# Performance work log

Hardware: AMD Instinct MI355X
Metric: run time of the kernel (lower is better)

Reference implementation:

```python
import jax, jax.numpy as jnp
import numpy as np

R = 0.2          # stable-distribution hash bucket width
TABLE_SIZE = 2   # hash table size (buckets)
M = 5            # number of appended ALSH transform dims
EPS = 1e-12


def conv2d(x, W, b, pad):
    out = jax.lax.conv_general_dilated(
        x, W, window_strides=(1, 1), padding=[(pad, pad), (pad, pad)],
        dimension_numbers=('NCHW', 'OIHW', 'NCHW'))
    return out + b[None, :, None, None]


def maxpool2(x):
    return jax.lax.reduce_window(x, -jnp.inf, jax.lax.max,
                                 (1, 1, 2, 2), (1, 1, 2, 2), 'VALID')


def alsh_mask(x, W, a, c):
    """ALSH filter selection: hash P(kernels) and Q(query) with a stable
    distribution hash h(v)=floor((a.v+b)/r) mod table_size; active filters
    are those landing in the query's bucket. Returns [B, Cout] 0/1 mask.
    Multiplying conv output by this mask == gather active filters then
    zero_fill_missing back to full channel count."""
    Cout, Cin, kH, kW = W.shape
    Kf = W.reshape(Cout, -1)                       # [Cout, Cin*kH*kW]
    norms = jnp.linalg.norm(Kf, axis=1)
    Kn = Kf / (jnp.max(norms) + EPS)               # scale so all norms <= 1
    n = jnp.linalg.norm(Kn, axis=1, keepdims=True)
    # P transform: append norm^2, norm^4, ..., norm^(2^M)
    powers = jnp.concatenate([n ** (2 ** (i + 1)) for i in range(M)], axis=1)
    P = jnp.concatenate([Kn, powers], axis=1)      # [Cout, d+M]
    kh = jnp.mod(jnp.floor((P @ a + c[0]) / R), TABLE_SIZE)  # [Cout]
    # query vector: per-sample channel means broadcast over kernel support
    cm = x.mean(axis=(2, 3))                       # [B, Cin]
    q = jnp.repeat(cm, kH * kW, axis=1)            # [B, Cin*kH*kW] (cin,kh,kw order)
    qn = q / (jnp.linalg.norm(q, axis=1, keepdims=True) + EPS)
    # Q transform: append M halves
    Qv = jnp.concatenate([qn, jnp.full((q.shape[0], M), 0.5, q.dtype)], axis=1)
    qh = jnp.mod(jnp.floor((Qv @ a + c[0]) / R), TABLE_SIZE)  # [B]
    return (kh[None, :] == qh[:, None]).astype(x.dtype)       # [B, Cout]


def setup_inputs() -> dict:
    key = jax.random.key(0)
    ks = jax.random.split(key, 16)
    u = lambda k, s: jax.random.uniform(k, s, jnp.float32, 0.0, R)
    n = lambda k, s, sc=0.1: jax.random.normal(k, s, jnp.float32) * sc
    return {
        'x': jax.random.normal(ks[0], (4096, 3, 32, 32), jnp.float32),
        'W1': n(ks[1], (16, 3, 5, 5)), 'b1': n(ks[2], (16,)),
        'a1': jax.random.normal(ks[3], (80,), jnp.float32), 'c1': u(ks[4], (1,)),
        'W2': n(ks[5], (20, 16, 5, 5)), 'b2': n(ks[6], (20,)),
        'a2': jax.random.normal(ks[7], (405,), jnp.float32), 'c2': u(ks[8], (1,)),
        'W3': n(ks[9], (20, 20, 5, 5)), 'b3': n(ks[10], (20,)),
        'a3': jax.random.normal(ks[11], (505,), jnp.float32), 'c3': u(ks[12], (1,)),
        'Wo': n(ks[13], (10, 320)), 'bo': n(ks[14], (10,)),
    }


def reference(x, W1, b1, a1, c1, W2, b2, a2, c2, W3, b3, a3, c3, Wo, bo):
    m1 = alsh_mask(x, W1, a1, c1)
    h = jax.nn.relu(conv2d(x, W1, b1, 2)) * m1[:, :, None, None]
    h = maxpool2(h)                                # [B,16,16,16]
    m2 = alsh_mask(h, W2, a2, c2)
    h = jax.nn.relu(conv2d(h, W2, b2, 2)) * m2[:, :, None, None]
    h = maxpool2(h)                                # [B,20,8,8]
    m3 = alsh_mask(h, W3, a3, c3)
    h = jax.nn.relu(conv2d(h, W3, b3, 2)) * m3[:, :, None, None]
    # zero_fill_missing -> identity here: inactive channels already zero
    h = maxpool2(h)                                # [B,20,4,4]
    flat = h.reshape(h.shape[0], -1)               # [B,320]
    return flat @ Wo.T + bo
```

## Files before the change

### kernel.cpp

```cpp
#include <hip/hip_runtime.h>
#include <hip/hip_bf16.h>

#define EPSV 1e-12
#define RHASH 0.2

__device__ __forceinline__ int fmod2(double t) {
    return (int)(((long long)floor(t)) & 1LL);
}

__device__ __forceinline__ void load_row6(const float* base, float* r) {
    float2 a0 = *(const float2*)(base);
    float2 a1 = *(const float2*)(base + 2);
    float2 a2 = *(const float2*)(base + 4);
    r[0] = a0.x; r[1] = a0.y; r[2] = a1.x; r[3] = a1.y; r[4] = a2.x; r[5] = a2.y;
}

__device__ void layer_setup(const float* W, const float* a, double cval,
                            int Co, int Ci, int* kh, double* asum, double* qc,
                            double* s_norm, float* Wbuf, float* abuf)
{
    const int t = threadIdx.x;
    const int D = Ci * 25;
    for (int i = t; i < Co * D; i += 256) Wbuf[i] = W[i];
    for (int i = t; i < D + 5; i += 256) abuf[i] = a[i];
    __syncthreads();
    if (t < Co) {
        double s = 0;
        for (int j = 0; j < D; ++j) { double w = (double)Wbuf[t * D + j]; s += w * w; }
        s_norm[t] = sqrt(s);
    }
    __syncthreads();
    if (t == 0) {
        double mx = 0;
        for (int i = 0; i < Co; ++i) mx = fmax(mx, s_norm[i]);
        s_norm[23] = 1.0 / (mx + EPSV);
    }
    __syncthreads();
    double scale = s_norm[23];
    if (t < Co) {
        double dp = 0;
        for (int j = 0; j < D; ++j) dp += (double)Wbuf[t * D + j] * (double)abuf[j];
        dp *= scale;
        double n = s_norm[t] * scale;
        double p = n * n;
        for (int m = 0; m < 5; ++m) { dp += p * (double)abuf[D + m]; p *= p; }
        kh[t] = fmod2((dp + cval) / RHASH);
    }
    if (t >= 64 && t < 64 + Ci) {
        int c = t - 64;
        double s = 0;
        for (int j = 0; j < 25; ++j) s += (double)abuf[c * 25 + j];
        asum[c] = s;
    }
    if (t == 128) {
        double s = 0;
        for (int m = 0; m < 5; ++m) s += (double)abuf[D + m];
        *qc = 0.5 * s + cval;
    }
    __syncthreads();
}

__global__ __launch_bounds__(256) void setup_kernel(
    const float* W1, const float* a1, const float* c1,
    const float* W2, const float* a2, const float* c2,
    const float* W3, const float* a3, const float* c3,
    double* dmeta, int* imeta)
{
    __shared__ float Wbuf[10000];
    __shared__ float abuf[512];
    __shared__ double s_norm[24];
    layer_setup(W1, a1, (double)c1[0], 16, 3,  imeta + 0,  dmeta + 0,  dmeta + 39, s_norm, Wbuf, abuf);
    layer_setup(W2, a2, (double)c2[0], 20, 16, imeta + 16, dmeta + 3,  dmeta + 40, s_norm, Wbuf, abuf);
    layer_setup(W3, a3, (double)c3[0], 20, 20, imeta + 36, dmeta + 19, dmeta + 41, s_norm, Wbuf, abuf);
}

__global__ __launch_bounds__(256) void pack_kernel(const float* W1, const float* W2, const float* W3,
                                                   float* Wp1, float* Wp2, float* Wp3)
{
    int i = blockIdx.x * 256 + threadIdx.x;
    if (i < 1200) {
        int co = i & 15, r = i >> 4;
        int kx = r % 5, r2 = r / 5, ky = r2 % 5, ci = r2 / 5;
        Wp1[i] = W1[co * 75 + ci * 25 + ky * 5 + kx];
    } else if (i < 1200 + 8960) {
        int k = i - 1200;
        int j = k % 28, r = k / 28;
        int cog = r % 4, r2 = r / 4, ky = r2 % 5, ci = r2 / 5;
        Wp2[k] = (j < 25) ? W2[(cog * 5 + j / 5) * 400 + ci * 25 + ky * 5 + (j % 5)] : 0.f;
    } else if (i < 1200 + 8960 + 11200) {
        int k = i - 10160;
        int j = k % 28, r = k / 28;
        int cog = r % 4, r2 = r / 4, ky = r2 % 5, ci = r2 / 5;
        Wp3[k] = (j < 25) ? W3[(cog * 5 + j / 5) * 500 + ci * 25 + ky * 5 + (j % 5)] : 0.f;
    }
}

__global__ __launch_bounds__(256) void conv1_kernel(
    const float* __restrict__ x, const float* __restrict__ Wp1,
    const float* __restrict__ b1, const int* __restrict__ kh1,
    const double* __restrict__ dmeta, float* __restrict__ h1,
    int* __restrict__ qh2)
{
    __shared__ float xs[3][36][38];
    __shared__ float Ws[1200];
    __shared__ double s_red[3];
    __shared__ double s_ch[16][4];

    const int b = blockIdx.x, t = threadIdx.x;
    const int w = t >> 6, ln = t & 63;

    for (int i = t; i < 3 * 36 * 38; i += 256) (&xs[0][0][0])[i] = 0.f;
    for (int i = t; i < 600; i += 256) ((float2*)Ws)[i] = ((const float2*)Wp1)[i];
    __syncthreads();
    const float2* xb2 = (const float2*)(x + (size_t)b * 3072);
    for (int i = t; i < 1536; i += 256) {
        int idx = i * 2, c = idx >> 10, rem = idx & 1023;
        *(float2*)&xs[c][(rem >> 5) + 2][(rem & 31) + 2] = xb2[i];
    }
    __syncthreads();

    if (w < 3) {
        double s = 0;
        for (int j = 0; j < 16; ++j) {
            int i = ln + 64 * j;
            s += (double)xs[w][(i >> 5) + 2][(i & 31) + 2];
        }
        #pragma unroll
        for (int off = 32; off; off >>= 1) s += __shfl_xor(s, off);
        if (ln == 0) s_red[w] = s;
    }
    __syncthreads();
    double dp = 0, nn = 0;
    #pragma unroll
    for (int c = 0; c < 3; ++c) {
        double cm = s_red[c] * (1.0 / 1024.0);
        dp += cm * dmeta[c]; nn += cm * cm;
    }
    const int qh = fmod2((dp / (5.0 * sqrt(nn) + EPSV) + dmeta[39]) / RHASH);

    const int py = t >> 4, px = t & 15;
    const int y0 = 2 * py, x0 = 2 * px;

    float acc[16][4];
    #pragma unroll
    for (int c = 0; c < 16; ++c) {
        float bb = b1[c];
        acc[c][0] = bb; acc[c][1] = bb; acc[c][2] = bb; acc[c][3] = bb;
    }
    #pragma unroll
    for (int ci = 0; ci < 3; ++ci) {
        float cur[6], nxt[6];
        load_row6(&xs[ci][y0][x0], cur);
        load_row6(&xs[ci][y0 + 1][x0], nxt);
        #pragma unroll
        for (int ky = 0; ky < 5; ++ky) {
            const float* wbase = Ws + ((ci * 5 + ky) * 5) * 16;
            #pragma unroll
            for (int kx = 0; kx < 5; ++kx) {
                float wc[16];
                const float4* wp = (const float4*)(wbase + kx * 16);
                *(float4*)&wc[0]  = wp[0];
                *(float4*)&wc[4]  = wp[1];
                *(float4*)&wc[8]  = wp[2];
                *(float4*)&wc[12] = wp[3];
                #pragma unroll
                for (int c = 0; c < 16; ++c) {
                    acc[c][0] = fmaf(wc[c], cur[kx],     acc[c][0]);
                    acc[c][1] = fmaf(wc[c], cur[kx + 1], acc[c][1]);
                    acc[c][2] = fmaf(wc[c], nxt[kx],     acc[c][2]);
                    acc[c][3] = fmaf(wc[c], nxt[kx + 1], acc[c][3]);
                }
            }
            if (ky < 4) {
                #pragma unroll
                for (int j = 0; j < 6; ++j) cur[j] = nxt[j];
                load_row6(&xs[ci][y0 + ky + 2][x0], nxt);
            }
        }
    }

    float mv[16];
    float* hb = h1 + (size_t)b * 4096 + t;
    #pragma unroll
    for (int c = 0; c < 16; ++c) {
        float m = fmaxf(fmaxf(acc[c][0], acc[c][1]), fmaxf(acc[c][2], acc[c][3]));
        mv[c] = fmaxf(m, 0.f) * ((kh1[c] == qh) ? 1.f : 0.f);
        hb[c * 256] = mv[c];
    }
    #pragma unroll
    for (int c = 0; c < 16; ++c) {
        double s = (double)mv[c];
        #pragma unroll
        for (int off = 32; off; off >>= 1) s += __shfl_xor(s, off);
        if (ln == 0) s_ch[c][w] = s;
    }
    __syncthreads();
    if (t == 0) {
        double dp2 = 0, nn2 = 0;
        #pragma unroll
        for (int c = 0; c < 16; ++c) {
            double cm = (s_ch[c][0] + s_ch[c][1] + s_ch[c][2] + s_ch[c][3]) * (1.0 / 256.0);
            dp2 += cm * dmeta[3 + c]; nn2 += cm * cm;
        }
        qh2[b] = fmod2((dp2 / (5.0 * sqrt(nn2) + EPSV) + dmeta[40]) / RHASH);
    }
}

__global__ __launch_bounds__(256) void conv2_kernel(
    const float* __restrict__ h1, const float* __restrict__ Wp2,
    const float* __restrict__ b2, const int* __restrict__ kh2,
    const int* __restrict__ qh2, const double* __restrict__ dmeta,
    float* __restrict__ h2, int* __restrict__ qh3)
{
    __shared__ float xs[8][20][22];
    __shared__ float Ws[4480];
    __shared__ double s_ch[20];

    const int b = blockIdx.x, t = threadIdx.x;
    const int cog = t >> 6, pos = t & 63;
    const int py = pos >> 3, px = pos & 7;
    const int y0 = 2 * py, x0 = 2 * px;

    for (int i = t; i < 8 * 20 * 22; i += 256) (&xs[0][0][0])[i] = 0.f;

    const int qh = qh2[b];
    float acc[5][4];
    #pragma unroll
    for (int c = 0; c < 5; ++c) {
        float bb = b2[cog * 5 + c];
        acc[c][0] = bb; acc[c][1] = bb; acc[c][2] = bb; acc[c][3] = bb;
    }
    __syncthreads();

    for (int ch = 0; ch < 2; ++ch) {
        for (int i = t; i < 2240; i += 256)
            ((float2*)Ws)[i] = ((const float2*)(Wp2 + ch * 4480))[i];
        const float2* src = (const float2*)(h1 + (size_t)b * 4096 + ch * 2048);
        for (int i = t; i < 1024; i += 256) {
            int ci = i >> 7, r = i & 127, p2 = r * 2;
            *(float2*)&xs[ci][(p2 >> 4) + 2][(p2 & 15) + 2] = src[i];
        }
        __syncthreads();

        for (int ci = 0; ci < 8; ++ci) {
            float cur[6], nxt[6];
            load_row6(&xs[ci][y0][x0], cur);
            load_row6(&xs[ci][y0 + 1][x0], nxt);
            #pragma unroll
            for (int ky = 0; ky < 5; ++ky) {
                float wv[28];
                const float4* wp = (const float4*)&Ws[((ci * 5 + ky) * 4 + cog) * 28];
                *(float4*)&wv[0]  = wp[0];
                *(float4*)&wv[4]  = wp[1];
                *(float4*)&wv[8]  = wp[2];
                *(float4*)&wv[12] = wp[3];
                *(float4*)&wv[16] = wp[4];
                *(float4*)&wv[20] = wp[5];
                *(float4*)&wv[24] = wp[6];
                #pragma unroll
                for (int c = 0; c < 5; ++c) {
                    #pragma unroll
                    for (int kx = 0; kx < 5; ++kx) {
                        float wgt = wv[c * 5 + kx];
                        acc[c][0] = fmaf(wgt, cur[kx],     acc[c][0]);
                        acc[c][1] = fmaf(wgt, cur[kx + 1], acc[c][1]);
                        acc[c][2] = fmaf(wgt, nxt[kx],     acc[c][2]);
                        acc[c][3] = fmaf(wgt, nxt[kx + 1], acc[c][3]);
                    }
                }
                if (ky < 4) {
                    #pragma unroll
                    for (int j = 0; j < 6; ++j) cur[j] = nxt[j];
                    load_row6(&xs[ci][y0 + ky + 2][x0], nxt);
                }
            }
        }
        __syncthreads();
    }

    float mv[5];
    float* ob = h2 + (size_t)b * 1280 + pos;
    #pragma unroll
    for (int c = 0; c < 5; ++c) {
        int co = cog * 5 + c;
        float m = fmaxf(fmaxf(acc[c][0], acc[c][1]), fmaxf(acc[c][2], acc[c][3]));
        mv[c] = fmaxf(m, 0.f) * ((kh2[co] == qh) ? 1.f : 0.f);
        ob[co * 64] = mv[c];
    }
    #pragma unroll
    for (int c = 0; c < 5; ++c) {
        double s = (double)mv[c];
        #pragma unroll
        for (int off = 32; off; off >>= 1) s += __shfl_xor(s, off);
        if (pos == 0) s_ch[cog * 5 + c] = s;
    }
    __syncthreads();
    if (t == 0) {
        double dp = 0, nn = 0;
        #pragma unroll
        for (int c = 0; c < 20; ++c) {
            double cm = s_ch[c] * (1.0 / 64.0);
            dp += cm * dmeta[19 + c]; nn += cm * cm;
        }
        qh3[b] = fmod2((dp / (5.0 * sqrt(nn) + EPSV) + dmeta[41]) / RHASH);
    }
}

__global__ __launch_bounds__(256) void conv3_kernel(
    const float* __restrict__ h2, const float* __restrict__ Wp3,
    const float* __restrict__ b3, const int* __restrict__ kh3,
    const int* __restrict__ qh3,
    const float* __restrict__ Wo, const float* __restrict__ bo,
    float* __restrict__ out, int B)
{
    __shared__ float xs[4][5][12][14];
    __shared__ float Ws[2800];
    __shared__ float flat[4][320];

    const int b0 = blockIdx.x * 4, t = threadIdx.x;
    const int s = t >> 6, q = t & 63, cog = q >> 4, pos = q & 15;
    const int py = pos >> 2, px = pos & 3;
    const int y0 = 2 * py, x0 = 2 * px;
    const int b = b0 + s;

    for (int i = t; i < 4 * 5 * 12 * 14; i += 256) (&xs[0][0][0][0])[i] = 0.f;

    const int qh = (b < B) ? qh3[b] : 0;
    float acc[5][4];
    #pragma unroll
    for (int c = 0; c < 5; ++c) {
        float bb = b3[cog * 5 + c];
        acc[c][0] = bb; acc[c][1] = bb; acc[c][2] = bb; acc[c][3] = bb;
    }
    __syncthreads();

    for (int ch = 0; ch < 4; ++ch) {
        for (int i = t; i < 1400; i += 256)
            ((float2*)Ws)[i] = ((const float2*)(Wp3 + ch * 2800))[i];
        for (int i = t; i < 640; i += 256) {
            int ss = i / 160, r = i - ss * 160, ci = r >> 5, rr = r & 31, p2 = rr * 2;
            if (b0 + ss < B)
                *(float2*)&xs[ss][ci][(p2 >> 3) + 2][(p2 & 7) + 2] =
                    ((const float2*)(h2 + (size_t)(b0 + ss) * 1280 + (ch * 5 + ci) * 64))[rr];
        }
        __syncthreads();

        #pragma unroll
        for (int ci = 0; ci < 5; ++ci) {
            float cur[6], nxt[6];
            load_row6(&xs[s][ci][y0][x0], cur);
            load_row6(&xs[s][ci][y0 + 1][x0], nxt);
            #pragma unroll
            for (int ky = 0; ky < 5; ++ky) {
                float wv[28];
                const float4* wp = (const float4*)&Ws[((ci * 5 + ky) * 4 + cog) * 28];
                *(float4*)&wv[0]  = wp[0];
                *(float4*)&wv[4]  = wp[1];
                *(float4*)&wv[8]  = wp[2];
                *(float4*)&wv[12] = wp[3];
                *(float4*)&wv[16] = wp[4];
                *(float4*)&wv[20] = wp[5];
                *(float4*)&wv[24] = wp[6];
                #pragma unroll
                for (int c = 0; c < 5; ++c) {
                    #pragma unroll
                    for (int kx = 0; kx < 5; ++kx) {
                        float wgt = wv[c * 5 + kx];
                        acc[c][0] = fmaf(wgt, cur[kx],     acc[c][0]);
                        acc[c][1] = fmaf(wgt, cur[kx + 1], acc[c][1]);
                        acc[c][2] = fmaf(wgt, nxt[kx],     acc[c][2]);
                        acc[c][3] = fmaf(wgt, nxt[kx + 1], acc[c][3]);
                    }
                }
                if (ky < 4) {
                    #pragma unroll
                    for (int j = 0; j < 6; ++j) cur[j] = nxt[j];
                    load_row6(&xs[s][ci][y0 + ky + 2][x0], nxt);
                }
            }
        }
        __syncthreads();
    }

    #pragma unroll
    for (int c = 0; c < 5; ++c) {
        int co = cog * 5 + c;
        float m = fmaxf(fmaxf(acc[c][0], acc[c][1]), fmaxf(acc[c][2], acc[c][3]));
        flat[s][co * 16 + pos] = fmaxf(m, 0.f) * ((kh3[co] == qh) ? 1.f : 0.f);
    }
    __syncthreads();

    if (t < 160) {
        const int g = t >> 2, qq = t & 3;
        const int ss = g / 10, o = g - ss * 10;
        float a = 0.f;
        const float* wr = Wo + o * 320;
        for (int k = qq; k < 320; k += 4) a = fmaf(flat[ss][k], wr[k], a);
        a += __shfl_xor(a, 1);
        a += __shfl_xor(a, 2);
        if (qq == 0 && b0 + ss < B) out[(size_t)(b0 + ss) * 10 + o] = a + bo[o];
    }
}

extern "C" void kernel_launch(void* const* d_in, const int* in_sizes, int n_in,
                              void* d_out, int out_size, void* d_ws, size_t ws_size,
                              hipStream_t stream)
{
    const float* x  = (const float*)d_in[0];
    const float* W1 = (const float*)d_in[1];
    const float* b1 = (const float*)d_in[2];
    const float* a1 = (const float*)d_in[3];
    const float* c1 = (const float*)d_in[4];
    const float* W2 = (const float*)d_in[5];
    const float* b2 = (const float*)d_in[6];
    const float* a2 = (const float*)d_in[7];
    const float* c2 = (const float*)d_in[8];
    const float* W3 = (const float*)d_in[9];
    const float* b3 = (const float*)d_in[10];
    const float* a3 = (const float*)d_in[11];
    const float* c3 = (const float*)d_in[12];
    const float* Wo = (const float*)d_in[13];
    const float* bo = (const float*)d_in[14];
    float* out = (float*)d_out;

    const int B = in_sizes[0] / 3072;

    float* h1  = (float*)d_ws;
    float* h2  = h1 + (size_t)B * 4096;
    float* Wp1 = h2 + (size_t)B * 1280;
    float* Wp2 = Wp1 + 1200;
    float* Wp3 = Wp2 + 8960;
    double* dmeta = (double*)(Wp3 + 11200);
    int* imeta = (int*)(dmeta + 42);
    int* qh2 = imeta + 56;
    int* qh3 = qh2 + B;

    setup_kernel<<<1, 256, 0, stream>>>(W1, a1, c1, W2, a2, c2, W3, a3, c3, dmeta, imeta);
    pack_kernel<<<84, 256, 0, stream>>>(W1, W2, W3, Wp1, Wp2, Wp3);
    conv1_kernel<<<B, 256, 0, stream>>>(x, Wp1, b1, imeta, dmeta, h1, qh2);
    conv2_kernel<<<B, 256, 0, stream>>>(h1, Wp2, b2, imeta + 16, qh2, dmeta, h2, qh3);
    conv3_kernel<<<(B + 3) / 4, 256, 0, stream>>>(h2, Wp3, b3, imeta + 36, qh3, Wo, bo, out, B);
}
```

Measured before the change: 567.3 us.

## Process two samples per conv2 block with wider per-thread output tiles

conv2 now handles two batch samples per block. Each thread computes two pooled positions (8 accumulators per output channel), so every weight vector read from shared memory feeds twice as many FMAs. Input channels are staged in four chunks of 4 instead of two of 8, and the per-sample channel-sum reduction is split into two 32-lane halves. Row padding in the shared tiles for conv1 and conv3 is also trimmed. The grid is halved to B/2, which assumes B is even and adds register pressure from the larger accumulator array.

```diff
diff --git a/kernel.cpp b/kernel.cpp
--- a/kernel.cpp
+++ b/kernel.cpp
@@ -101,7 +101,7 @@
     const double* __restrict__ dmeta, float* __restrict__ h1,
     int* __restrict__ qh2)
 {
-    __shared__ float xs[3][36][38];
+    __shared__ float xs[3][36][36];
     __shared__ float Ws[1200];
     __shared__ double s_red[3];
     __shared__ double s_ch[16][4];
@@ -109,7 +109,7 @@
     const int b = blockIdx.x, t = threadIdx.x;
     const int w = t >> 6, ln = t & 63;
 
-    for (int i = t; i < 3 * 36 * 38; i += 256) (&xs[0][0][0])[i] = 0.f;
+    for (int i = t; i < 3 * 36 * 36; i += 256) (&xs[0][0][0])[i] = 0.f;
     for (int i = t; i < 600; i += 256) ((float2*)Ws)[i] = ((const float2*)Wp1)[i];
     __syncthreads();
     const float2* xb2 = (const float2*)(x + (size_t)b * 3072);
@@ -212,40 +212,44 @@
     const int* __restrict__ qh2, const double* __restrict__ dmeta,
     float* __restrict__ h2, int* __restrict__ qh3)
 {
-    __shared__ float xs[8][20][22];
-    __shared__ float Ws[4480];
-    __shared__ double s_ch[20];
-
-    const int b = blockIdx.x, t = threadIdx.x;
-    const int cog = t >> 6, pos = t & 63;
-    const int py = pos >> 3, px = pos & 7;
-    const int y0 = 2 * py, x0 = 2 * px;
-
-    for (int i = t; i < 8 * 20 * 22; i += 256) (&xs[0][0][0])[i] = 0.f;
-
-    const int qh = qh2[b];
-    float acc[5][4];
+    __shared__ float xs[2][4][20][20];
+    __shared__ float Ws[2240];
+    __shared__ double s_ch[2][20];
+
+    const int b0 = blockIdx.x * 2, t = threadIdx.x;
+    const int cog = t >> 6, slot = t & 63;
+    const int s = slot >> 5, py = (slot >> 2) & 7, pxp = slot & 3;
+    const int y0 = 2 * py, x0a = 2 * pxp, x0b = 2 * pxp + 8;
+
+    for (int i = t; i < 3200; i += 256) (&xs[0][0][0][0])[i] = 0.f;
+
+    const int qh = qh2[b0 + s];
+    float acc[5][8];
     #pragma unroll
     for (int c = 0; c < 5; ++c) {
         float bb = b2[cog * 5 + c];
-        acc[c][0] = bb; acc[c][1] = bb; acc[c][2] = bb; acc[c][3] = bb;
-    }
-    __syncthreads();
-
-    for (int ch = 0; ch < 2; ++ch) {
-        for (int i = t; i < 2240; i += 256)
-            ((float2*)Ws)[i] = ((const float2*)(Wp2 + ch * 4480))[i];
-        const float2* src = (const float2*)(h1 + (size_t)b * 4096 + ch * 2048);
+        #pragma unroll
+        for (int j = 0; j < 8; ++j) acc[c][j] = bb;
+    }
+    __syncthreads();
+
+    for (int ch = 0; ch < 4; ++ch) {
+        for (int i = t; i < 1120; i += 256)
+            ((float2*)Ws)[i] = ((const float2*)(Wp2 + ch * 2240))[i];
         for (int i = t; i < 1024; i += 256) {
-            int ci = i >> 7, r = i & 127, p2 = r * 2;
-            *(float2*)&xs[ci][(p2 >> 4) + 2][(p2 & 15) + 2] = src[i];
+            int ss = i >> 9, r = i & 511, ci = r >> 7, rr = r & 127, p2 = rr * 2;
+            *(float2*)&xs[ss][ci][(p2 >> 4) + 2][(p2 & 15) + 2] =
+                ((const float2*)(h1 + (size_t)(b0 + ss) * 4096 + (ch * 4 + ci) * 256))[rr];
         }
         __syncthreads();
 
-        for (int ci = 0; ci < 8; ++ci) {
-            float cur[6], nxt[6];
-            load_row6(&xs[ci][y0][x0], cur);
-            load_row6(&xs[ci][y0 + 1][x0], nxt);
+        #pragma unroll
+        for (int ci = 0; ci < 4; ++ci) {
+            float ca[6], na[6], cb[6], nb[6];
+            load_row6(&xs[s][ci][y0][x0a], ca);
+            load_row6(&xs[s][ci][y0 + 1][x0a], na);
+            load_row6(&xs[s][ci][y0][x0b], cb);
+            load_row6(&xs[s][ci][y0 + 1][x0b], nb);
             #pragma unroll
             for (int ky = 0; ky < 5; ++ky) {
                 float wv[28];
@@ -262,47 +266,57 @@
                     #pragma unroll
                     for (int kx = 0; kx < 5; ++kx) {
                         float wgt = wv[c * 5 + kx];
-                        acc[c][0] = fmaf(wgt, cur[kx],     acc[c][0]);
-                        acc[c][1] = fmaf(wgt, cur[kx + 1], acc[c][1]);
-                        acc[c][2] = fmaf(wgt, nxt[kx],     acc[c][2]);
-                        acc[c][3] = fmaf(wgt, nxt[kx + 1], acc[c][3]);
+                        acc[c][0] = fmaf(wgt, ca[kx],     acc[c][0]);
+                        acc[c][1] = fmaf(wgt, ca[kx + 1], acc[c][1]);
+                        acc[c][2] = fmaf(wgt, na[kx],     acc[c][2]);
+                        acc[c][3] = fmaf(wgt, na[kx + 1], acc[c][3]);
+                        acc[c][4] = fmaf(wgt, cb[kx],     acc[c][4]);
+                        acc[c][5] = fmaf(wgt, cb[kx + 1], acc[c][5]);
+                        acc[c][6] = fmaf(wgt, nb[kx],     acc[c][6]);
+                        acc[c][7] = fmaf(wgt, nb[kx + 1], acc[c][7]);
                     }
                 }
                 if (ky < 4) {
                     #pragma unroll
-                    for (int j = 0; j < 6; ++j) cur[j] = nxt[j];
-                    load_row6(&xs[ci][y0 + ky + 2][x0], nxt);
+                    for (int j = 0; j < 6; ++j) { ca[j] = na[j]; cb[j] = nb[j]; }
+                    load_row6(&xs[s][ci][y0 + ky + 2][x0a], na);
+                    load_row6(&xs[s][ci][y0 + ky + 2][x0b], nb);
                 }
             }
         }
         __syncthreads();
     }
 
-    float mv[5];
-    float* ob = h2 + (size_t)b * 1280 + pos;
+    float* ob = h2 + (size_t)(b0 + s) * 1280 + py * 8 + pxp;
+    double csum[5];
     #pragma unroll
     for (int c = 0; c < 5; ++c) {
         int co = cog * 5 + c;
-        float m = fmaxf(fmaxf(acc[c][0], acc[c][1]), fmaxf(acc[c][2], acc[c][3]));
-        mv[c] = fmaxf(m, 0.f) * ((kh2[co] == qh) ? 1.f : 0.f);
-        ob[co * 64] = mv[c];
+        float mask = (kh2[co] == qh) ? 1.f : 0.f;
+        float mA = fmaxf(fmaxf(acc[c][0], acc[c][1]), fmaxf(acc[c][2], acc[c][3]));
+        float mB = fmaxf(fmaxf(acc[c][4], acc[c][5]), fmaxf(acc[c][6], acc[c][7]));
+        float vA = fmaxf(mA, 0.f) * mask;
+        float vB = fmaxf(mB, 0.f) * mask;
+        ob[co * 64]     = vA;
+        ob[co * 64 + 4] = vB;
+        csum[c] = (double)vA + (double)vB;
     }
     #pragma unroll
     for (int c = 0; c < 5; ++c) {
-        double s = (double)mv[c];
-        #pragma unroll
-        for (int off = 32; off; off >>= 1) s += __shfl_xor(s, off);
-        if (pos == 0) s_ch[cog * 5 + c] = s;
-    }
-    __syncthreads();
-    if (t == 0) {
-        double dp = 0, nn = 0;
+        double sv = csum[c];
+        #pragma unroll
+        for (int off = 16; off; off >>= 1) sv += __shfl_xor(sv, off);
+        if ((slot & 31) == 0) s_ch[s][cog * 5 + c] = sv;
+    }
+    __syncthreads();
+    if (t < 2) {
+        double dp2 = 0, nn2 = 0;
         #pragma unroll
         for (int c = 0; c < 20; ++c) {
-            double cm = s_ch[c] * (1.0 / 64.0);
-            dp += cm * dmeta[19 + c]; nn += cm * cm;
-        }
-        qh3[b] = fmod2((dp / (5.0 * sqrt(nn) + EPSV) + dmeta[41]) / RHASH);
+            double cm = s_ch[t][c] * (1.0 / 64.0);
+            dp2 += cm * dmeta[19 + c]; nn2 += cm * cm;
+        }
+        qh3[b0 + t] = fmod2((dp2 / (5.0 * sqrt(nn2) + EPSV) + dmeta[41]) / RHASH);
     }
 }
 
@@ -313,7 +327,7 @@
     const float* __restrict__ Wo, const float* __restrict__ bo,
     float* __restrict__ out, int B)
 {
-    __shared__ float xs[4][5][12][14];
+    __shared__ float xs[4][5][12][12];
     __shared__ float Ws[2800];
     __shared__ float flat[4][320];
 
@@ -323,7 +337,7 @@
     const int y0 = 2 * py, x0 = 2 * px;
     const int b = b0 + s;
 
-    for (int i = t; i < 4 * 5 * 12 * 14; i += 256) (&xs[0][0][0][0])[i] = 0.f;
+    for (int i = t; i < 4 * 5 * 144; i += 256) (&xs[0][0][0][0])[i] = 0.f;
 
     const int qh = (b < B) ? qh3[b] : 0;
     float acc[5][4];
@@ -438,6 +452,6 @@
     setup_kernel<<<1, 256, 0, stream>>>(W1, a1, c1, W2, a2, c2, W3, a3, c3, dmeta, imeta);
     pack_kernel<<<84, 256, 0, stream>>>(W1, W2, W3, Wp1, Wp2, Wp3);
     conv1_kernel<<<B, 256, 0, stream>>>(x, Wp1, b1, imeta, dmeta, h1, qh2);
-    conv2_kernel<<<B, 256, 0, stream>>>(h1, Wp2, b2, imeta + 16, qh2, dmeta, h2, qh3);
+    conv2_kernel<<<B / 2, 256, 0, stream>>>(h1, Wp2, b2, imeta + 16, qh2, dmeta, h2, qh3);
     conv3_kernel<<<(B + 3) / 4, 256, 0, stream>>>(h2, Wp3, b3, imeta + 36, qh3, Wo, bo, out, B);
 }
```

New measurement: 572.8 us. No clear change (+1.0%).
